# Performance work log

Measured on AMD Instinct MI355X. Metric: run time of the kernel, lower is better.

The kernel has to match this reference:

```python
import jax, jax.numpy as jnp
import numpy as np

B, N, DIM, H, DH = 4, 2048, 1024, 16, 64
SCALE = DH ** -0.5


def rotate_half(x):
    x1, x2 = jnp.split(x, 2, axis=-1)
    return jnp.concatenate((-x2, x1), axis=-1)


def apply_rope(pos, t):
    # pos: [n, d] broadcast over [b, h, n, d]
    return t * jnp.cos(pos) + rotate_half(t) * jnp.sin(pos)


def setup_inputs() -> dict:
    key = jax.random.key(0)
    ks = jax.random.split(key, 5)
    inner = H * DH
    return {
        "x": jax.random.normal(ks[0], (B, N, DIM), dtype=jnp.float32),
        "rotary_emb_x": jax.random.normal(ks[1], (N, DH), dtype=jnp.float32),
        "Wq": jax.random.normal(ks[2], (DIM, inner), dtype=jnp.float32) * (DIM ** -0.5),
        "Wkv": jax.random.normal(ks[3], (DIM, 2 * inner), dtype=jnp.float32) * (DIM ** -0.5),
        "Wo": jax.random.normal(ks[4], (inner, DIM), dtype=jnp.float32) * (inner ** -0.5),
        "bo": jnp.zeros((DIM,), dtype=jnp.float32),
    }


def reference(x, rotary_emb_x, Wq, Wkv, Wo, bo):
    # projections (self-attention: context = x)
    q = x @ Wq                      # [b, n, h*d]
    kv = x @ Wkv                    # [b, n, 2*h*d]
    k, v = jnp.split(kv, 2, axis=-1)

    def to_heads(t):
        b, n, _ = t.shape
        return t.reshape(b, n, H, DH).transpose(0, 2, 1, 3)  # [b, h, n, d]

    q, k, v = map(to_heads, (q, k, v))

    # rotary on q and k (no context => both use rotary_emb_x)
    q = apply_rope(rotary_emb_x, q)
    k = apply_rope(rotary_emb_x, k)

    # scaled dot-product attention
    scores = jnp.einsum("bhnd,bhmd->bhnm", q, k) * SCALE
    attn = jax.nn.softmax(scores, axis=-1)
    out = jnp.einsum("bhnm,bhmd->bhnd", attn, v)  # [b, h, n, d]

    out = out.transpose(0, 2, 1, 3).reshape(x.shape[0], x.shape[1], H * DH)
    return out @ Wo + bo
```

## Files before the change

kernel.cpp:

```cpp
#include <hip/hip_runtime.h>
#include <hip/hip_bf16.h>
#include <stdint.h>

typedef __attribute__((ext_vector_type(4))) float f32x4;
typedef __attribute__((ext_vector_type(8))) short s16x8;
typedef __attribute__((ext_vector_type(4))) unsigned short u16x4;
typedef __attribute__((ext_vector_type(2))) uint32_t u32x2;

__device__ __forceinline__ unsigned short f2bf(float f) {
  union { float f; uint32_t u; } v; v.f = f;
  uint32_t r = v.u + 0x7fffu + ((v.u >> 16) & 1u);
  return (unsigned short)(r >> 16);
}

__device__ __forceinline__ void load_lds16(const void* g, void* l) {
  __builtin_amdgcn_global_load_lds(
      (const __attribute__((address_space(1))) void*)g,
      (__attribute__((address_space(3))) void*)l, 16, 0, 0);
}

#define MFMA16(a, b, c) __builtin_amdgcn_mfma_f32_16x16x32_bf16((a), (b), (c), 0, 0, 0)

__global__ void k_cvt(const float* __restrict__ in, unsigned short* __restrict__ out, int n4) {
  int i = blockIdx.x * blockDim.x + threadIdx.x;
  int stride = gridDim.x * blockDim.x;
  for (; i < n4; i += stride) {
    f32x4 v = ((const f32x4*)in)[i];
    u16x4 o;
    o[0] = f2bf(v[0]); o[1] = f2bf(v[1]); o[2] = f2bf(v[2]); o[3] = f2bf(v[3]);
    ((u16x4*)out)[i] = o;
  }
}

__global__ __launch_bounds__(256) void k_transpose(const float* __restrict__ in,
    unsigned short* __restrict__ out, int K, int N) {
  __shared__ float t[32][33];
  const int tx = threadIdx.x, ty = threadIdx.y;
  const int n0 = blockIdx.x * 32, k0 = blockIdx.y * 32;
#pragma unroll
  for (int i = 0; i < 32; i += 8) t[ty + i][tx] = in[(size_t)(k0 + ty + i) * N + n0 + tx];
  __syncthreads();
#pragma unroll
  for (int i = 0; i < 32; i += 8) out[(size_t)(n0 + ty + i) * K + k0 + tx] = f2bf(t[tx][ty + i]);
}

__global__ __launch_bounds__(256) void k_gemm_qkv(const unsigned short* __restrict__ A,
    const unsigned short* __restrict__ Bt, const float* __restrict__ rope,
    unsigned short* __restrict__ qw, unsigned short* __restrict__ kw,
    unsigned short* __restrict__ vt) {
  __shared__ unsigned short As[128 * 64];
  __shared__ unsigned short Bs[128 * 64];
  const int tid = threadIdx.x, l = tid & 63, w = tid >> 6;
  const int tm = blockIdx.y, tn = blockIdx.x;
  const int wr = (w >> 1) * 64, wc = (w & 1) * 64;
  const int lg = l >> 4, lr = l & 15;
  f32x4 acc[4][4] = {};

  for (int kt = 0; kt < 16; ++kt) {
    if (kt) __syncthreads();
    const int k0 = kt * 64;
#pragma unroll
    for (int is = 0; is < 4; ++is) {
      int off = is * 4096 + w * 1024 + l * 16;
      int row = off >> 7;
      int kk = (off & 127) >> 1;
      load_lds16(A + (size_t)(tm * 128 + row) * 1024 + k0 + kk, (char*)As + off);
      load_lds16(Bt + (size_t)(tn * 128 + row) * 1024 + k0 + kk, (char*)Bs + off);
    }
    __syncthreads();
#pragma unroll
    for (int ks = 0; ks < 2; ++ks) {
      s16x8 af[4], bf[4];
#pragma unroll
      for (int mi = 0; mi < 4; ++mi)
        af[mi] = *(const s16x8*)&As[(wr + mi * 16 + lr) * 64 + ks * 32 + lg * 8];
#pragma unroll
      for (int ni = 0; ni < 4; ++ni)
        bf[ni] = *(const s16x8*)&Bs[(wc + ni * 16 + lr) * 64 + ks * 32 + lg * 8];
#pragma unroll
      for (int mi = 0; mi < 4; ++mi)
#pragma unroll
        for (int ni = 0; ni < 4; ++ni)
          acc[mi][ni] = MFMA16(af[mi], bf[ni], acc[mi][ni]);
    }
  }

  const int c0 = tn * 128 + wc;
  const int tensor = c0 >> 10;
  const int h = (c0 & 1023) >> 6;
  if (tensor < 2) {
    unsigned short* dst = tensor == 0 ? qw : kw;
#pragma unroll
    for (int mi = 0; mi < 4; ++mi) {
#pragma unroll
      for (int reg = 0; reg < 4; ++reg) {
        int m = tm * 128 + wr + mi * 16 + lg * 4 + reg;
        int b = m >> 11, n = m & 2047;
        size_t base = ((size_t)(b * 16 + h) * 2048 + n) * 64;
#pragma unroll
        for (int ni = 0; ni < 4; ++ni) {
          int d = ni * 16 + lr;
          float val = acc[mi][ni][reg];
          float partner = acc[mi][ni ^ 2][reg];
          float p = rope[n * 64 + d];
          float sn, cs; __sincosf(p, &sn, &cs);
          dst[base + d] = f2bf(val * cs + (d < 32 ? -partner : partner) * sn);
        }
      }
    }
  } else {
#pragma unroll
    for (int mi = 0; mi < 4; ++mi) {
      int m0 = tm * 128 + wr + mi * 16 + lg * 4;
      int b = m0 >> 11, n0 = m0 & 2047;
#pragma unroll
      for (int ni = 0; ni < 4; ++ni) {
        int d = ni * 16 + lr;
        u16x4 vv;
#pragma unroll
        for (int reg = 0; reg < 4; ++reg) vv[reg] = f2bf(acc[mi][ni][reg]);
        *(u16x4*)(vt + ((size_t)(b * 16 + h) * 64 + d) * 2048 + n0) = vv;
      }
    }
  }
}

__global__ __launch_bounds__(256, 4) void k_attn(const unsigned short* __restrict__ qw,
    const unsigned short* __restrict__ kw, const unsigned short* __restrict__ vt,
    unsigned short* __restrict__ aout) {
  __shared__ unsigned short Kl[64 * 64];
  __shared__ unsigned short Vl[64 * 64];
  __shared__ unsigned short Pl[4][32 * 64];
  const int tid = threadIdx.x, l = tid & 63, w = tid >> 6;
  const int lg = l >> 4, lr = l & 15;
  const int bh = blockIdx.y;
  const int qb = blockIdx.x * 128 + w * 32;
  const size_t hbase = (size_t)bh * 2048 * 64;
  unsigned short* Pw = Pl[w];
  const float c1 = 0.18033688011112042f;

  s16x8 qf[2][2];
#pragma unroll
  for (int qi = 0; qi < 2; ++qi)
#pragma unroll
    for (int ks = 0; ks < 2; ++ks)
      qf[qi][ks] = *(const s16x8*)(qw + hbase + (size_t)(qb + qi * 16 + lr) * 64 + ks * 32 + lg * 8);

  f32x4 o[2][4] = {};
  float m2[2] = {-1e30f, -1e30f};
  float lsum[2] = {0.f, 0.f};

  for (int kv0 = 0; kv0 < 2048; kv0 += 64) {
    __syncthreads();
#pragma unroll
    for (int i = 0; i < 2; ++i) {
      int off = i * 4096 + tid * 16;
      int row = off >> 7, cb = off & 127;
      int g = (cb ^ ((row & 7) << 4)) >> 1;
      load_lds16(kw + hbase + (size_t)(kv0 + row) * 64 + g, (char*)Kl + off);
      load_lds16(vt + hbase + (size_t)row * 2048 + kv0 + g, (char*)Vl + off);
    }
    __syncthreads();

    f32x4 s[2][4];
#pragma unroll
    for (int qi = 0; qi < 2; ++qi)
#pragma unroll
      for (int ni = 0; ni < 4; ++ni) { f32x4 z = {0.f, 0.f, 0.f, 0.f}; s[qi][ni] = z; }
#pragma unroll
    for (int ks = 0; ks < 2; ++ks) {
#pragma unroll
      for (int ni = 0; ni < 4; ++ni) {
        int r = ni * 16 + lr;
        s16x8 kf = *(const s16x8*)((const char*)Kl + r * 128 + ((ks * 64 + lg * 16) ^ ((r & 7) << 4)));
#pragma unroll
        for (int qi = 0; qi < 2; ++qi)
          s[qi][ni] = MFMA16(kf, qf[qi][ks], s[qi][ni]);
      }
    }

#pragma unroll
    for (int qi = 0; qi < 2; ++qi) {
      float mloc = s[qi][0][0];
#pragma unroll
      for (int ni = 0; ni < 4; ++ni)
#pragma unroll
        for (int r = 0; r < 4; ++r) mloc = fmaxf(mloc, s[qi][ni][r]);
      mloc = fmaxf(mloc, __shfl_xor(mloc, 16));
      mloc = fmaxf(mloc, __shfl_xor(mloc, 32));
      float m2new = fmaxf(m2[qi], mloc * c1);
      float sf = exp2f(m2[qi] - m2new);
      m2[qi] = m2new;
      float ls = 0.f;
#pragma unroll
      for (int ni = 0; ni < 4; ++ni)
#pragma unroll
        for (int r = 0; r < 4; ++r) {
          float p = exp2f(fmaf(s[qi][ni][r], c1, -m2new));
          s[qi][ni][r] = p;
          ls += p;
        }
      ls += __shfl_xor(ls, 16);
      ls += __shfl_xor(ls, 32);
      lsum[qi] = lsum[qi] * sf + ls;
#pragma unroll
      for (int ni = 0; ni < 4; ++ni) {
        uint32_t p01, p23;
        asm("v_cvt_pk_bf16_f32 %0, %1, %2" : "=v"(p01) : "v"(s[qi][ni][0]), "v"(s[qi][ni][1]));
        asm("v_cvt_pk_bf16_f32 %0, %1, %2" : "=v"(p23) : "v"(s[qi][ni][2]), "v"(s[qi][ni][3]));
        int row = qi * 16 + lr;
        int cbyte = (ni * 32 + lg * 8) ^ ((lr & 7) << 4);
        u32x2 pp = {p01, p23};
        *(u32x2*)((char*)Pw + row * 128 + cbyte) = pp;
      }
      float sfb[4];
#pragma unroll
      for (int r = 0; r < 4; ++r) sfb[r] = __shfl(sf, lg * 4 + r);
#pragma unroll
      for (int nd = 0; nd < 4; ++nd)
#pragma unroll
        for (int r = 0; r < 4; ++r) o[qi][nd][r] *= sfb[r];
    }

#pragma unroll
    for (int ks = 0; ks < 2; ++ks) {
#pragma unroll
      for (int qi = 0; qi < 2; ++qi) {
        int row = qi * 16 + lr;
        s16x8 af = *(const s16x8*)((const char*)Pw + row * 128 + ((ks * 64 + lg * 16) ^ ((row & 7) << 4)));
#pragma unroll
        for (int nd = 0; nd < 4; ++nd) {
          int rv = nd * 16 + lr;
          s16x8 vf = *(const s16x8*)((const char*)Vl + rv * 128 + ((ks * 64 + lg * 16) ^ ((rv & 7) << 4)));
          o[qi][nd] = MFMA16(af, vf, o[qi][nd]);
        }
      }
    }
  }

  const int b = bh >> 4, h = bh & 15;
#pragma unroll
  for (int qi = 0; qi < 2; ++qi) {
    float inv = 1.f / lsum[qi];
    float invb[4];
#pragma unroll
    for (int r = 0; r < 4; ++r) invb[r] = __shfl(inv, lg * 4 + r);
#pragma unroll
    for (int r = 0; r < 4; ++r) {
      int n = qb + qi * 16 + lg * 4 + r;
      size_t ob = ((size_t)(b * 2048 + n) * 16 + h) * 64;
#pragma unroll
      for (int nd = 0; nd < 4; ++nd)
        aout[ob + nd * 16 + lr] = f2bf(o[qi][nd][r] * invb[r]);
    }
  }
}

__global__ __launch_bounds__(256) void k_gemm_out(const unsigned short* __restrict__ A,
    const unsigned short* __restrict__ Bt, const float* __restrict__ bo,
    float* __restrict__ out) {
  __shared__ unsigned short As[128 * 64];
  __shared__ unsigned short Bs[128 * 64];
  const int tid = threadIdx.x, l = tid & 63, w = tid >> 6;
  const int tm = blockIdx.y, tn = blockIdx.x;
  const int wr = (w >> 1) * 64, wc = (w & 1) * 64;
  const int lg = l >> 4, lr = l & 15;
  f32x4 acc[4][4] = {};

  for (int kt = 0; kt < 16; ++kt) {
    if (kt) __syncthreads();
    const int k0 = kt * 64;
#pragma unroll
    for (int is = 0; is < 4; ++is) {
      int off = is * 4096 + w * 1024 + l * 16;
      int row = off >> 7;
      int kk = (off & 127) >> 1;
      load_lds16(A + (size_t)(tm * 128 + row) * 1024 + k0 + kk, (char*)As + off);
      load_lds16(Bt + (size_t)(tn * 128 + row) * 1024 + k0 + kk, (char*)Bs + off);
    }
    __syncthreads();
#pragma unroll
    for (int ks = 0; ks < 2; ++ks) {
      s16x8 af[4], bf[4];
#pragma unroll
      for (int mi = 0; mi < 4; ++mi)
        af[mi] = *(const s16x8*)&As[(wr + mi * 16 + lr) * 64 + ks * 32 + lg * 8];
#pragma unroll
      for (int ni = 0; ni < 4; ++ni)
        bf[ni] = *(const s16x8*)&Bs[(wc + ni * 16 + lr) * 64 + ks * 32 + lg * 8];
#pragma unroll
      for (int mi = 0; mi < 4; ++mi)
#pragma unroll
        for (int ni = 0; ni < 4; ++ni)
          acc[mi][ni] = MFMA16(af[mi], bf[ni], acc[mi][ni]);
    }
  }
  const int c0 = tn * 128 + wc;
#pragma unroll
  for (int mi = 0; mi < 4; ++mi)
#pragma unroll
    for (int reg = 0; reg < 4; ++reg) {
      int m = tm * 128 + wr + mi * 16 + lg * 4 + reg;
#pragma unroll
      for (int ni = 0; ni < 4; ++ni) {
        int c = c0 + ni * 16 + lr;
        out[(size_t)m * 1024 + c] = acc[mi][ni][reg] + bo[c];
      }
    }
}

extern "C" void kernel_launch(void* const* d_in, const int* in_sizes, int n_in,
                              void* d_out, int out_size, void* d_ws, size_t ws_size,
                              hipStream_t stream) {
  const float* x    = (const float*)d_in[0];
  const float* rope = (const float*)d_in[1];
  const float* Wq   = (const float*)d_in[2];
  const float* Wkv  = (const float*)d_in[3];
  const float* Wo   = (const float*)d_in[4];
  const float* bo   = (const float*)d_in[5];
  float* out = (float*)d_out;

  unsigned short* ws  = (unsigned short*)d_ws;
  unsigned short* xb  = ws;
  unsigned short* wt  = xb + 8192 * 1024;
  unsigned short* wot = wt + 3072 * 1024;
  unsigned short* qws = wot + 1024 * 1024;
  unsigned short* kws = qws + 64 * 2048 * 64;
  unsigned short* vtw = kws + 64 * 2048 * 64;
  unsigned short* aws = xb;

  k_cvt<<<1024, 256, 0, stream>>>(x, xb, 8192 * 1024 / 4);
  dim3 tb(32, 8);
  k_transpose<<<dim3(32, 32), tb, 0, stream>>>(Wq, wt, 1024, 1024);
  k_transpose<<<dim3(64, 32), tb, 0, stream>>>(Wkv, wt + 1024 * 1024, 1024, 2048);
  k_transpose<<<dim3(32, 32), tb, 0, stream>>>(Wo, wot, 1024, 1024);

  k_gemm_qkv<<<dim3(24, 64), 256, 0, stream>>>(xb, wt, rope, qws, kws, vtw);
  k_attn<<<dim3(16, 64), 256, 0, stream>>>(qws, kws, vtw, aws);
  k_gemm_out<<<dim3(8, 64), 256, 0, stream>>>(aws, wot, bo, out);
}
```

Before: 364.7 us.

## Double-buffer attention K/V, precompute rope table, lazy softmax rescale

New measurement: 343.5 us. -5.8%, faster.

```diff
diff --git a/kernel.cpp b/kernel.cpp
--- a/kernel.cpp
+++ b/kernel.cpp
@@ -3,6 +3,7 @@
 #include <stdint.h>
 
 typedef __attribute__((ext_vector_type(4))) float f32x4;
+typedef __attribute__((ext_vector_type(2))) float f32x2;
 typedef __attribute__((ext_vector_type(8))) short s16x8;
 typedef __attribute__((ext_vector_type(4))) unsigned short u16x4;
 typedef __attribute__((ext_vector_type(2))) uint32_t u32x2;
@@ -32,6 +33,17 @@
   }
 }
 
+__global__ __launch_bounds__(256) void k_rope_tab(const float* __restrict__ rope,
+    float* __restrict__ tq, float* __restrict__ tk) {
+  int i = blockIdx.x * blockDim.x + threadIdx.x;
+  float p = rope[i];
+  float sn, cs; __sincosf(p, &sn, &cs);
+  f32x2 a = {cs * 0.125f, sn * 0.125f};
+  f32x2 b = {cs, sn};
+  ((f32x2*)tq)[i] = a;
+  ((f32x2*)tk)[i] = b;
+}
+
 __global__ __launch_bounds__(256) void k_transpose(const float* __restrict__ in,
     unsigned short* __restrict__ out, int K, int N) {
   __shared__ float t[32][33];
@@ -45,7 +57,8 @@
 }
 
 __global__ __launch_bounds__(256) void k_gemm_qkv(const unsigned short* __restrict__ A,
-    const unsigned short* __restrict__ Bt, const float* __restrict__ rope,
+    const unsigned short* __restrict__ Bt, const float* __restrict__ tq,
+    const float* __restrict__ tk,
     unsigned short* __restrict__ qw, unsigned short* __restrict__ kw,
     unsigned short* __restrict__ vt) {
   __shared__ unsigned short As[128 * 64];
@@ -90,6 +103,7 @@
   const int h = (c0 & 1023) >> 6;
   if (tensor < 2) {
     unsigned short* dst = tensor == 0 ? qw : kw;
+    const float* tbl = tensor == 0 ? tq : tk;
 #pragma unroll
     for (int mi = 0; mi < 4; ++mi) {
 #pragma unroll
@@ -97,14 +111,14 @@
         int m = tm * 128 + wr + mi * 16 + lg * 4 + reg;
         int b = m >> 11, n = m & 2047;
         size_t base = ((size_t)(b * 16 + h) * 2048 + n) * 64;
+        const float* tb = tbl + (size_t)n * 128;
 #pragma unroll
         for (int ni = 0; ni < 4; ++ni) {
           int d = ni * 16 + lr;
+          f32x2 cssn = *(const f32x2*)(tb + 2 * d);
           float val = acc[mi][ni][reg];
           float partner = acc[mi][ni ^ 2][reg];
-          float p = rope[n * 64 + d];
-          float sn, cs; __sincosf(p, &sn, &cs);
-          dst[base + d] = f2bf(val * cs + (d < 32 ? -partner : partner) * sn);
+          dst[base + d] = f2bf(val * cssn[0] + (d < 32 ? -partner : partner) * cssn[1]);
         }
       }
     }
@@ -128,16 +142,16 @@
 __global__ __launch_bounds__(256, 4) void k_attn(const unsigned short* __restrict__ qw,
     const unsigned short* __restrict__ kw, const unsigned short* __restrict__ vt,
     unsigned short* __restrict__ aout) {
-  __shared__ unsigned short Kl[64 * 64];
-  __shared__ unsigned short Vl[64 * 64];
-  __shared__ unsigned short Pl[4][32 * 64];
+  __shared__ unsigned short Kl[2][64 * 64];
+  __shared__ unsigned short Vl[2][64 * 64];
+  __shared__ unsigned short Pl[4][16 * 64];
   const int tid = threadIdx.x, l = tid & 63, w = tid >> 6;
   const int lg = l >> 4, lr = l & 15;
   const int bh = blockIdx.y;
   const int qb = blockIdx.x * 128 + w * 32;
   const size_t hbase = (size_t)bh * 2048 * 64;
   unsigned short* Pw = Pl[w];
-  const float c1 = 0.18033688011112042f;
+  const float LOG2E = 1.4426950408889634f;
 
   s16x8 qf[2][2];
 #pragma unroll
@@ -146,114 +160,117 @@
     for (int ks = 0; ks < 2; ++ks)
       qf[qi][ks] = *(const s16x8*)(qw + hbase + (size_t)(qb + qi * 16 + lr) * 64 + ks * 32 + lg * 8);
 
+  s16x8 vone;
+#pragma unroll
+  for (int j = 0; j < 8; ++j) vone[j] = (short)0x3F80;
+
   f32x4 o[2][4] = {};
+  f32x4 lacc[2] = {};
   float m2[2] = {-1e30f, -1e30f};
-  float lsum[2] = {0.f, 0.f};
-
-  for (int kv0 = 0; kv0 < 2048; kv0 += 64) {
-    __syncthreads();
+
+  auto STAGE = [&](int kv0, int buf) {
 #pragma unroll
     for (int i = 0; i < 2; ++i) {
       int off = i * 4096 + tid * 16;
       int row = off >> 7, cb = off & 127;
       int g = (cb ^ ((row & 7) << 4)) >> 1;
-      load_lds16(kw + hbase + (size_t)(kv0 + row) * 64 + g, (char*)Kl + off);
-      load_lds16(vt + hbase + (size_t)row * 2048 + kv0 + g, (char*)Vl + off);
-    }
-    __syncthreads();
-
+      load_lds16(kw + hbase + (size_t)(kv0 + row) * 64 + g, (char*)Kl[buf] + off);
+      load_lds16(vt + hbase + (size_t)row * 2048 + kv0 + g, (char*)Vl[buf] + off);
+    }
+  };
+
+  auto COMPUTE = [&](const unsigned short* Kc, const unsigned short* Vc) {
     f32x4 s[2][4];
 #pragma unroll
     for (int qi = 0; qi < 2; ++qi)
 #pragma unroll
       for (int ni = 0; ni < 4; ++ni) { f32x4 z = {0.f, 0.f, 0.f, 0.f}; s[qi][ni] = z; }
-#pragma unroll
-    for (int ks = 0; ks < 2; ++ks) {
+    __builtin_amdgcn_s_setprio(1);
+#pragma unroll
+    for (int ks = 0; ks < 2; ++ks)
 #pragma unroll
       for (int ni = 0; ni < 4; ++ni) {
         int r = ni * 16 + lr;
-        s16x8 kf = *(const s16x8*)((const char*)Kl + r * 128 + ((ks * 64 + lg * 16) ^ ((r & 7) << 4)));
-#pragma unroll
-        for (int qi = 0; qi < 2; ++qi)
-          s[qi][ni] = MFMA16(kf, qf[qi][ks], s[qi][ni]);
-      }
-    }
-
+        s16x8 kf = *(const s16x8*)((const char*)Kc + r * 128 + ((ks * 64 + lg * 16) ^ ((r & 7) << 4)));
+        s[0][ni] = MFMA16(kf, qf[0][ks], s[0][ni]);
+        s[1][ni] = MFMA16(kf, qf[1][ks], s[1][ni]);
+      }
+    __builtin_amdgcn_s_setprio(0);
 #pragma unroll
     for (int qi = 0; qi < 2; ++qi) {
-      float mloc = s[qi][0][0];
-#pragma unroll
-      for (int ni = 0; ni < 4; ++ni)
-#pragma unroll
-        for (int r = 0; r < 4; ++r) mloc = fmaxf(mloc, s[qi][ni][r]);
+      float m01 = fmaxf(fmaxf(s[qi][0][0], s[qi][0][1]), fmaxf(s[qi][0][2], s[qi][0][3]));
+      float m11 = fmaxf(fmaxf(s[qi][1][0], s[qi][1][1]), fmaxf(s[qi][1][2], s[qi][1][3]));
+      float m21 = fmaxf(fmaxf(s[qi][2][0], s[qi][2][1]), fmaxf(s[qi][2][2], s[qi][2][3]));
+      float m31 = fmaxf(fmaxf(s[qi][3][0], s[qi][3][1]), fmaxf(s[qi][3][2], s[qi][3][3]));
+      float mloc = fmaxf(fmaxf(m01, m11), fmaxf(m21, m31));
       mloc = fmaxf(mloc, __shfl_xor(mloc, 16));
       mloc = fmaxf(mloc, __shfl_xor(mloc, 32));
-      float m2new = fmaxf(m2[qi], mloc * c1);
-      float sf = exp2f(m2[qi] - m2new);
-      m2[qi] = m2new;
-      float ls = 0.f;
-#pragma unroll
-      for (int ni = 0; ni < 4; ++ni)
-#pragma unroll
-        for (int r = 0; r < 4; ++r) {
-          float p = exp2f(fmaf(s[qi][ni][r], c1, -m2new));
-          s[qi][ni][r] = p;
-          ls += p;
-        }
-      ls += __shfl_xor(ls, 16);
-      ls += __shfl_xor(ls, 32);
-      lsum[qi] = lsum[qi] * sf + ls;
+      float g2 = mloc * LOG2E;
+      if (!__all(g2 <= m2[qi] + 8.f)) {
+        float m2n = fmaxf(m2[qi], g2);
+        float sf = exp2f(m2[qi] - m2n);
+        m2[qi] = m2n;
+        float sfb[4];
+#pragma unroll
+        for (int r2 = 0; r2 < 4; ++r2) sfb[r2] = __shfl(sf, lg * 4 + r2);
+#pragma unroll
+        for (int nd = 0; nd < 4; ++nd)
+#pragma unroll
+          for (int r2 = 0; r2 < 4; ++r2) o[qi][nd][r2] *= sfb[r2];
+#pragma unroll
+        for (int r2 = 0; r2 < 4; ++r2) lacc[qi][r2] *= sfb[r2];
+      }
+      const float mq = m2[qi];
 #pragma unroll
       for (int ni = 0; ni < 4; ++ni) {
+#pragma unroll
+        for (int r2 = 0; r2 < 4; ++r2)
+          s[qi][ni][r2] = exp2f(fmaf(s[qi][ni][r2], LOG2E, -mq));
         uint32_t p01, p23;
         asm("v_cvt_pk_bf16_f32 %0, %1, %2" : "=v"(p01) : "v"(s[qi][ni][0]), "v"(s[qi][ni][1]));
         asm("v_cvt_pk_bf16_f32 %0, %1, %2" : "=v"(p23) : "v"(s[qi][ni][2]), "v"(s[qi][ni][3]));
-        int row = qi * 16 + lr;
-        int cbyte = (ni * 32 + lg * 8) ^ ((lr & 7) << 4);
         u32x2 pp = {p01, p23};
-        *(u32x2*)((char*)Pw + row * 128 + cbyte) = pp;
-      }
-      float sfb[4];
-#pragma unroll
-      for (int r = 0; r < 4; ++r) sfb[r] = __shfl(sf, lg * 4 + r);
-#pragma unroll
-      for (int nd = 0; nd < 4; ++nd)
-#pragma unroll
-        for (int r = 0; r < 4; ++r) o[qi][nd][r] *= sfb[r];
-    }
-
-#pragma unroll
-    for (int ks = 0; ks < 2; ++ks) {
-#pragma unroll
-      for (int qi = 0; qi < 2; ++qi) {
-        int row = qi * 16 + lr;
-        s16x8 af = *(const s16x8*)((const char*)Pw + row * 128 + ((ks * 64 + lg * 16) ^ ((row & 7) << 4)));
+        *(u32x2*)((char*)Pw + lr * 128 + ((ni * 32 + lg * 8) ^ ((lr & 7) << 4))) = pp;
+      }
+      __builtin_amdgcn_s_setprio(1);
+#pragma unroll
+      for (int ks = 0; ks < 2; ++ks) {
+        s16x8 pa = *(const s16x8*)((const char*)Pw + lr * 128 + ((ks * 64 + lg * 16) ^ ((lr & 7) << 4)));
+        lacc[qi] = MFMA16(pa, vone, lacc[qi]);
 #pragma unroll
         for (int nd = 0; nd < 4; ++nd) {
           int rv = nd * 16 + lr;
-          s16x8 vf = *(const s16x8*)((const char*)Vl + rv * 128 + ((ks * 64 + lg * 16) ^ ((rv & 7) << 4)));
-          o[qi][nd] = MFMA16(af, vf, o[qi][nd]);
+          s16x8 vf = *(const s16x8*)((const char*)Vc + rv * 128 + ((ks * 64 + lg * 16) ^ ((rv & 7) << 4)));
+          o[qi][nd] = MFMA16(pa, vf, o[qi][nd]);
         }
       }
-    }
+      __builtin_amdgcn_s_setprio(0);
+    }
+  };
+
+  STAGE(0, 0);
+  __syncthreads();
+  for (int t = 0; t < 32; t += 2) {
+    if (t + 1 < 32) STAGE((t + 1) * 64, 1);
+    COMPUTE(Kl[0], Vl[0]);
+    __syncthreads();
+    if (t + 2 < 32) STAGE((t + 2) * 64, 0);
+    COMPUTE(Kl[1], Vl[1]);
+    __syncthreads();
   }
 
   const int b = bh >> 4, h = bh & 15;
 #pragma unroll
-  for (int qi = 0; qi < 2; ++qi) {
-    float inv = 1.f / lsum[qi];
-    float invb[4];
-#pragma unroll
-    for (int r = 0; r < 4; ++r) invb[r] = __shfl(inv, lg * 4 + r);
-#pragma unroll
-    for (int r = 0; r < 4; ++r) {
-      int n = qb + qi * 16 + lg * 4 + r;
+  for (int qi = 0; qi < 2; ++qi)
+#pragma unroll
+    for (int r2 = 0; r2 < 4; ++r2) {
+      float inv = 1.f / lacc[qi][r2];
+      int n = qb + qi * 16 + lg * 4 + r2;
       size_t ob = ((size_t)(b * 2048 + n) * 16 + h) * 64;
 #pragma unroll
       for (int nd = 0; nd < 4; ++nd)
-        aout[ob + nd * 16 + lr] = f2bf(o[qi][nd][r] * invb[r]);
-    }
-  }
+        aout[ob + nd * 16 + lr] = f2bf(o[qi][nd][r2] * inv);
+    }
 }
 
 __global__ __launch_bounds__(256) void k_gemm_out(const unsigned short* __restrict__ A,
@@ -327,15 +344,18 @@
   unsigned short* qws = wot + 1024 * 1024;
   unsigned short* kws = qws + 64 * 2048 * 64;
   unsigned short* vtw = kws + 64 * 2048 * 64;
+  float* tq = (float*)(vtw + 64 * 2048 * 64);
+  float* tk = tq + 2048 * 64 * 2;
   unsigned short* aws = xb;
 
   k_cvt<<<1024, 256, 0, stream>>>(x, xb, 8192 * 1024 / 4);
+  k_rope_tab<<<512, 256, 0, stream>>>(rope, tq, tk);
   dim3 tb(32, 8);
   k_transpose<<<dim3(32, 32), tb, 0, stream>>>(Wq, wt, 1024, 1024);
   k_transpose<<<dim3(64, 32), tb, 0, stream>>>(Wkv, wt + 1024 * 1024, 1024, 2048);
   k_transpose<<<dim3(32, 32), tb, 0, stream>>>(Wo, wot, 1024, 1024);
 
-  k_gemm_qkv<<<dim3(24, 64), 256, 0, stream>>>(xb, wt, rope, qws, kws, vtw);
+  k_gemm_qkv<<<dim3(24, 64), 256, 0, stream>>>(xb, wt, tq, tk, qws, kws, vtw);
   k_attn<<<dim3(16, 64), 256, 0, stream>>>(qws, kws, vtw, aws);
   k_gemm_out<<<dim3(8, 64), 256, 0, stream>>>(aws, wot, bo, out);
 }
```
